# Kernel optimization log

Measured on AMD Instinct MI355X. Metric: run time of the kernel, lower is better.

## Reference

```python
import jax, jax.numpy as jnp
import numpy as np

EPS = 1e-6


def setup_inputs() -> dict:
    key = jax.random.key(0)
    ks = jax.random.split(key, 10)
    N1, N2, K, E, LAYERS = 4096, 4096, 10, 262144, 3
    D = 2 ** K  # 1024
    us = jax.random.uniform(ks[0], (LAYERS, N1, D), dtype=jnp.float32)
    vs = jax.random.uniform(ks[1], (LAYERS, N2, D), dtype=jnp.float32)
    gamma = jax.random.normal(ks[2], (N1, LAYERS), dtype=jnp.float32)
    delta = jax.random.normal(ks[3], (N2, LAYERS), dtype=jnp.float32)
    latent_z1 = jax.random.uniform(ks[4], (N1, LAYERS), dtype=jnp.float32)
    latent_w1 = jax.random.uniform(ks[5], (N2, LAYERS), dtype=jnp.float32)
    # p_k_l initialized as log(uniform) in torch; any real values are valid params
    p_ks = jnp.full((LAYERS, K + 1), jnp.log(1.0 / (K + 1)), dtype=jnp.float32)
    p_ks = p_ks + 0.01 * jax.random.normal(ks[6], (LAYERS, K + 1), dtype=jnp.float32)
    L_ = 5.0 * jnp.ones((1,), dtype=jnp.float32)
    sparse_is = jax.random.randint(ks[7], (LAYERS, E), 0, N1, dtype=jnp.int64) if jax.config.jax_enable_x64 else jax.random.randint(ks[7], (LAYERS, E), 0, N1).astype(jnp.int32)
    sparse_js = jax.random.randint(ks[8], (LAYERS, E), 0, N2).astype(sparse_is.dtype)
    return {"us": us, "vs": vs, "gamma": gamma, "delta": delta,
            "latent_z1": latent_z1, "latent_w1": latent_w1,
            "p_ks": p_ks, "L_": L_,
            "sparse_is": sparse_is, "sparse_js": sparse_js}


def reference(us, vs, gamma, delta, latent_z1, latent_w1, p_ks, L_, sparse_is, sparse_js):
    LAYERS, N1, D = us.shape
    N2 = vs.shape[1]
    K = p_ks.shape[1] - 1  # tree_height
    latent_z = jax.nn.softmax(latent_z1, axis=1)  # Softmax(dim=1)
    latent_w = jax.nn.softmax(latent_w1, axis=1)
    L = jax.nn.softplus(L_)[0]
    ll = jnp.float32(0.0)
    for layer in range(LAYERS):
        p_k = jax.nn.softmax(p_ks[layer], axis=0)  # soft_0
        g = gamma[:, layer]                         # [N1]
        d = delta[:, layer]                         # [N2]
        emb_z = jax.nn.softmax(us[layer], axis=1)   # [N1, D]
        emb_w = jax.nn.softmax(vs[layer], axis=1)   # [N2, D]
        # hierarchical tree-weighted similarity: sum of GEMMs at coarsening levels
        inter = p_k[0] * jnp.ones((N1, N2), dtype=us.dtype)
        z_k, w_k = emb_z, emb_w
        for k in range(1, K):
            z_k = z_k.reshape(N1, -1, 2).sum(axis=2)  # [N1, D/2^k]
            w_k = w_k.reshape(N2, -1, 2).sum(axis=2)  # [N2, D/2^k]
            inter = inter + p_k[k] * jnp.einsum('nd,md->nm', z_k, w_k + EPS)
        inter = inter + p_k[K] * jnp.einsum('nd,md->nm', emb_z, emb_w + EPS)
        mat_1 = g[:, None] + d[None, :]                              # [N1, N2]
        mat_0 = (latent_z[:, layer][:, None] * L) * (latent_w[:, layer] + EPS)[None, :] * inter
        mat = jax.nn.softplus(mat_0 + mat_1)
        z_pdist1 = mat.sum()
        if N1 == N2:  # remove diagonal contributions
            z_pdist1 = z_pdist1 - jnp.trace(mat)
        i_ = sparse_is[layer]
        j_ = sparse_js[layer]
        z_pdist2 = (mat_0[i_, j_] + mat_1[i_, j_]).sum()
        ll = ll + (z_pdist2 - z_pdist1)
    return ll
```

## Files before the change

kernel.cpp:

```cpp
#include <hip/hip_runtime.h>
#include <hip/hip_bf16.h>
#include <stdint.h>

#define EPSV 1e-6f
#define N1 4096
#define N2 4096
#define DD 1024
#define NLAYERS 3
#define KKC 10

typedef __bf16 bf16_t;
typedef __bf16 bf16x8 __attribute__((ext_vector_type(8)));
typedef float f32x4 __attribute__((ext_vector_type(4)));
typedef long longx2 __attribute__((ext_vector_type(2)));

#define ZSCALE 256.0f
#define WSCALE 64.0f
#define INVSCALE 6.103515625e-05f

#define NBIN_L 1024
#define NBIN_T (NLAYERS*NBIN_L)

__device__ __forceinline__ float softplus_fast(float x) {
  return fmaxf(x, 0.f) + __logf(1.f + __expf(-fabsf(x)));
}
__device__ __forceinline__ float softplus_ref(float x) {
  return fmaxf(x, 0.f) + log1pf(expf(-fabsf(x)));
}
__device__ __forceinline__ float wredsum(float x) {
  #pragma unroll
  for (int o = 32; o; o >>= 1) x += __shfl_xor(x, o, 64);
  return x;
}
__device__ __forceinline__ float wredmax(float x) {
  #pragma unroll
  for (int o = 32; o; o >>= 1) x = fmaxf(x, __shfl_xor(x, o, 64));
  return x;
}
__device__ __forceinline__ void global_load_lds16(const void* g, void* l) {
  __builtin_amdgcn_global_load_lds(
      (const __attribute__((address_space(1))) uint32_t*)g,
      (__attribute__((address_space(3))) uint32_t*)l, 16, 0, 0);
}

__device__ __forceinline__ uint32_t enc_e4m3(float x) {
  if (x < 0.015625f) return (uint32_t)__float2int_rn(x * 512.0f);
  uint32_t u = __float_as_uint(x);
  u += 0x7FFFFu + ((u >> 20) & 1u);
  return (((u >> 23) - 120u) << 3) | ((u >> 20) & 7u);
}

__global__ __launch_bounds__(256) void prep_small(
    const float* __restrict__ lz, const float* __restrict__ lw,
    const float* __restrict__ gamma, const float* __restrict__ delta,
    const float* __restrict__ pks, const float* __restrict__ Lp,
    float* __restrict__ consts, float* __restrict__ a_tab, float* __restrict__ b_tab,
    float* __restrict__ g_tab, float* __restrict__ d_tab,
    uint32_t* __restrict__ hist, float* __restrict__ out)
{
  int n = blockIdx.x * blockDim.x + threadIdx.x;
  float Lv = softplus_ref(Lp[0]);
  if (n == 0) out[0] = 0.f;
  if (n < NBIN_T) hist[n] = 0u;
  if (n < N1) {
    float z0 = lz[n*3], z1 = lz[n*3+1], z2 = lz[n*3+2];
    float m = fmaxf(z0, fmaxf(z1, z2));
    float e0 = expf(z0-m), e1 = expf(z1-m), e2 = expf(z2-m);
    float inv = 1.f/(e0+e1+e2);
    a_tab[0*N1+n] = e0*inv*Lv; a_tab[1*N1+n] = e1*inv*Lv; a_tab[2*N1+n] = e2*inv*Lv;
    float w0 = lw[n*3], w1 = lw[n*3+1], w2 = lw[n*3+2];
    m = fmaxf(w0, fmaxf(w1, w2));
    e0 = expf(w0-m); e1 = expf(w1-m); e2 = expf(w2-m);
    inv = 1.f/(e0+e1+e2);
    b_tab[0*N2+n] = e0*inv+EPSV; b_tab[1*N2+n] = e1*inv+EPSV; b_tab[2*N2+n] = e2*inv+EPSV;
    #pragma unroll
    for (int k = 0; k < 3; ++k) {
      g_tab[k*N1+n] = gamma[n*3+k];
      d_tab[k*N2+n] = delta[n*3+k];
    }
  }
  if (n < NLAYERS) {
    float p[KKC+1]; float m = -1e30f;
    for (int k = 0; k <= KKC; ++k) { p[k] = pks[n*(KKC+1)+k]; m = fmaxf(m, p[k]); }
    float s = 0.f;
    for (int k = 0; k <= KKC; ++k) { p[k] = expf(p[k]-m); s += p[k]; }
    float inv = 1.f/s;
    for (int k = 0; k <= KKC; ++k) consts[8 + n*(KKC+1) + k] = p[k]*inv;
    consts[n] = p[0]*inv + EPSV*(1.f - p[0]*inv);
  }
}

#define EPB 2048

__global__ __launch_bounds__(256) void edge_hist(
    const int* __restrict__ is_, const int* __restrict__ js_,
    uint32_t* __restrict__ hist, int E)
{
  __shared__ uint32_t h[NBIN_L];
  const int lay = blockIdx.y;
  const int t = threadIdx.x;
  #pragma unroll
  for (int i = 0; i < NBIN_L/256; ++i) h[t + i*256] = 0u;
  __syncthreads();
  const int e0 = blockIdx.x * EPB;
  const int e1 = min(e0 + EPB, E);
  for (int e = e0 + t; e < e1; e += 256) {
    int i = is_[(size_t)lay*E + e], j = js_[(size_t)lay*E + e];
    atomicAdd(&h[(i>>7)*32 + (j>>7)], 1u);
  }
  __syncthreads();
  #pragma unroll
  for (int i = 0; i < NBIN_L/256; ++i)
    if (h[t + i*256]) atomicAdd(&hist[lay*NBIN_L + t + i*256], h[t + i*256]);
}

__global__ __launch_bounds__(256) void edge_scan(
    const uint32_t* __restrict__ hist, uint32_t* __restrict__ off,
    uint32_t* __restrict__ cursor, int E)
{
  __shared__ uint32_t sa[NBIN_L], sb[NBIN_L];
  const int lay = blockIdx.x;
  const int t = threadIdx.x;
  const uint32_t base = (uint32_t)lay * (uint32_t)E;
  for (int i = t; i < NBIN_L; i += 256) sa[i] = hist[lay*NBIN_L + i];
  __syncthreads();
  uint32_t* src = sa; uint32_t* dst = sb;
  for (int s = 1; s < NBIN_L; s <<= 1) {
    for (int i = t; i < NBIN_L; i += 256) dst[i] = src[i] + (i >= s ? src[i-s] : 0u);
    __syncthreads();
    uint32_t* tmp = src; src = dst; dst = tmp;
  }
  for (int i = t; i < NBIN_L; i += 256) {
    uint32_t ex = base + (i ? src[i-1] : 0u);
    off[lay*NBIN_L + i] = ex; cursor[lay*NBIN_L + i] = ex;
  }
  if (t == 0 && lay == NLAYERS-1) off[NBIN_T] = base + src[NBIN_L-1];
}

__global__ __launch_bounds__(256) void edge_scatter(
    const int* __restrict__ is_, const int* __restrict__ js_,
    uint32_t* __restrict__ cursor, uint16_t* __restrict__ ebuf, int E)
{
  __shared__ uint32_t h[NBIN_L];
  __shared__ uint32_t basev[NBIN_L];
  const int lay = blockIdx.y;
  const int t = threadIdx.x;
  #pragma unroll
  for (int i = 0; i < NBIN_L/256; ++i) h[t + i*256] = 0u;
  __syncthreads();
  const int e0 = blockIdx.x * EPB;
  const int e1 = min(e0 + EPB, E);
  for (int e = e0 + t; e < e1; e += 256) {
    int i = is_[(size_t)lay*E + e], j = js_[(size_t)lay*E + e];
    atomicAdd(&h[(i>>7)*32 + (j>>7)], 1u);
  }
  __syncthreads();
  #pragma unroll
  for (int i = 0; i < NBIN_L/256; ++i) {
    int b = t + i*256;
    basev[b] = h[b] ? atomicAdd(&cursor[lay*NBIN_L + b], h[b]) : 0u;
    h[b] = 0u;
  }
  __syncthreads();
  for (int e = e0 + t; e < e1; e += 256) {
    int i = is_[(size_t)lay*E + e], j = js_[(size_t)lay*E + e];
    int b = (i>>7)*32 + (j>>7);
    uint32_t r = atomicAdd(&h[b], 1u);
    ebuf[basev[b] + r] = (uint16_t)(((i & 127) << 7) | (j & 127));
  }
}

__global__ __launch_bounds__(256) void prep_rows(
    const float* __restrict__ us, const float* __restrict__ vs,
    uint8_t* __restrict__ zt8, uint8_t* __restrict__ wt8, size_t lstride,
    const float* __restrict__ consts, int layer0)
{
  const int t = threadIdx.x, w = t >> 6, l = t & 63;
  const int n = blockIdx.x*4 + w;
  const int layer = layer0 + blockIdx.y;
  const int zmode = (blockIdx.z == 0);
  const float* src = (zmode ? us : vs) + ((size_t)layer*N1 + n)*DD + l*16;
  uint8_t* drow = (zmode ? zt8 : wt8) + (size_t)blockIdx.y*lstride + (size_t)n*1024;
  const int p0 = (l>>2)*64 + ((l&1)*2)*16 + ((l&3)>>1)*8;

  float e[16];
  {
    const float4* s4 = (const float4*)src;
    float4 u0 = s4[0], u1 = s4[1], u2 = s4[2], u3 = s4[3];
    e[0]=u0.x; e[1]=u0.y; e[2]=u0.z; e[3]=u0.w;
    e[4]=u1.x; e[5]=u1.y; e[6]=u1.z; e[7]=u1.w;
    e[8]=u2.x; e[9]=u2.y; e[10]=u2.z; e[11]=u2.w;
    e[12]=u3.x; e[13]=u3.y; e[14]=u3.z; e[15]=u3.w;
  }
  float mx = e[0];
  #pragma unroll
  for (int i = 1; i < 16; ++i) mx = fmaxf(mx, e[i]);
  mx = wredmax(mx);
  float s = 0.f;
  #pragma unroll
  for (int i = 0; i < 16; ++i) { e[i] = __expf(e[i]-mx); s += e[i]; }
  s = wredsum(s);
  float inv = 1.f/s;
  #pragma unroll
  for (int i = 0; i < 16; ++i) e[i] *= inv;

  uint32_t b4[4] = {0u, 0u, 0u, 0u};
  if (!zmode) {
    #pragma unroll
    for (int i = 0; i < 16; ++i)
      b4[i>>2] |= enc_e4m3(e[i]*WSCALE) << ((i&3)*8);
  } else {
    float s1[8], s2[4], s3[2], s4v;
    #pragma unroll
    for (int i = 0; i < 8; ++i) s1[i] = e[2*i] + e[2*i+1];
    #pragma unroll
    for (int i = 0; i < 4; ++i) s2[i] = s1[2*i] + s1[2*i+1];
    s3[0] = s2[0]+s2[1]; s3[1] = s2[2]+s2[3];
    s4v = s3[0]+s3[1];
    float s5 = s4v + __shfl_xor(s4v, 1, 64);
    float s6 = s5  + __shfl_xor(s5, 2, 64);
    float s7 = s6  + __shfl_xor(s6, 4, 64);
    float s8 = s7  + __shfl_xor(s7, 8, 64);
    float s9 = s8  + __shfl_xor(s8, 16, 64);
    const float* pk = consts + 8 + layer*(KKC+1);
    const float base = pk[4]*s4v + pk[5]*s5 + pk[6]*s6 + pk[7]*s7 + pk[8]*s8 + pk[9]*s9;
    const float p1 = pk[1], p2 = pk[2], p3 = pk[3], p10 = pk[10];
    #pragma unroll
    for (int i = 0; i < 16; ++i) {
      float v = p10*e[i] + p1*s1[i>>1] + p2*s2[i>>2] + p3*s3[i>>3] + base;
      b4[i>>2] |= enc_e4m3(v*ZSCALE) << ((i&3)*8);
    }
  }
  uint64_t u0 = (uint64_t)b4[0] | ((uint64_t)b4[1] << 32);
  uint64_t u1 = (uint64_t)b4[2] | ((uint64_t)b4[3] << 32);
  *(uint64_t*)(drow + p0)      = u0;
  *(uint64_t*)(drow + p0 + 16) = u1;
}

__global__ __launch_bounds__(256, 4) void gemm_fused(
    const uint8_t* __restrict__ Az8, size_t zls,
    const uint8_t* __restrict__ Bw8, size_t wls,
    const float* __restrict__ a_tab, const float* __restrict__ b_tab,
    const float* __restrict__ g_tab, const float* __restrict__ d_tab,
    const float* __restrict__ consts, int layer0,
    const uint32_t* __restrict__ eoff, const uint16_t* __restrict__ ebuf,
    float* __restrict__ out)
{
  extern __shared__ char lds[];
  const int t = threadIdx.x;
  const int w = t >> 6, l = t & 63;
  const int wm = w >> 1, wn = w & 1;
  const int fr = l & 15, fq = l >> 4;

  const int nbx = gridDim.x, nby = gridDim.y;
  int lid = blockIdx.x + nbx*(blockIdx.y + nby*blockIdx.z);
  const int nblk = nbx*nby*gridDim.z;
  const int cpx = nblk >> 3;
  int nid = (lid & 7)*cpx + (lid >> 3);
  const int bz = nid / (nbx*nby);
  const int rem = nid % (nbx*nby);
  const int bi = rem % nbx, bj = rem / nbx;

  const int i0 = bi*128, j0 = bj*128;
  const int layer = layer0 + bz;
  Az8 += (size_t)bz*zls + (size_t)i0*1024;
  Bw8 += (size_t)bz*wls + (size_t)j0*1024;

  f32x4 acc[4][4];
  f32x4 zero = {0.f, 0.f, 0.f, 0.f};
  #pragma unroll
  for (int m = 0; m < 4; ++m)
    #pragma unroll
    for (int nn = 0; nn < 4; ++nn) acc[m][nn] = zero;

  const int go = (l & 7) ^ (l >> 3);
  const size_t s_off = (size_t)((l >> 3)*2 + (go >> 2))*1024 + (size_t)(go & 3)*16;
  const int slot = (((fr & 1) << 2) + fq) ^ (fr >> 1);
  const int abase = wm*4096 + (fr>>1)*128 + slot*16;
  const int bbase = 8192 + wn*4096 + (fr>>1)*128 + slot*16;

  longx2 ar2[4], br2[4];

#define STG_A(tile) do { \
    char* _d = lds + ((tile)&1)*16384 + w*2048; \
    const uint8_t* _s = Az8 + (size_t)(w*32)*1024 + (size_t)(tile)*64 + s_off; \
    global_load_lds16(_s, _d); \
    global_load_lds16(_s + (size_t)16*1024, _d + 1024); \
  } while (0)
#define STG_B(tile) do { \
    char* _d = lds + ((tile)&1)*16384 + 8192 + w*2048; \
    const uint8_t* _s = Bw8 + (size_t)(w*32)*1024 + (size_t)(tile)*64 + s_off; \
    global_load_lds16(_s, _d); \
    global_load_lds16(_s + (size_t)16*1024, _d + 1024); \
  } while (0)

  STG_A(0); STG_B(0);

  for (int u = 0; u < 16; ++u) {
    const int cb = (u & 1)*16384;
    asm volatile("s_waitcnt vmcnt(0)" ::: "memory");
    asm volatile("s_barrier" ::: "memory");
    #pragma unroll
    for (int i = 0; i < 4; ++i)
      ar2[i] = *(const longx2*)(lds + cb + abase + i*1024);
    #pragma unroll
    for (int j = 0; j < 4; ++j)
      br2[j] = *(const longx2*)(lds + cb + bbase + j*1024);
    if (u < 15) { STG_A(u+1); STG_B(u+1); }
    __builtin_amdgcn_s_setprio(1);
    #pragma unroll
    for (int i = 0; i < 4; ++i)
      #pragma unroll
      for (int j = 0; j < 4; ++j) {
        acc[i][j] = __builtin_amdgcn_mfma_f32_16x16x32_fp8_fp8(
            ar2[i].x, br2[j].x, acc[i][j], 0, 0, 0);
        acc[i][j] = __builtin_amdgcn_mfma_f32_16x16x32_fp8_fp8(
            ar2[i].y, br2[j].y, acc[i][j], 0, 0, 0);
      }
    __builtin_amdgcn_s_setprio(0);
  }
#undef STG_A
#undef STG_B

  __syncthreads();
  const float cc = consts[layer];
  {
    char* cbase = lds + wm*16384 + fq*1024 + wn*128 + fr*2;
    #pragma unroll
    for (int m = 0; m < 4; ++m)
      #pragma unroll
      for (int nn = 0; nn < 4; ++nn)
        #pragma unroll
        for (int r = 0; r < 4; ++r)
          *(bf16_t*)(cbase + m*4096 + r*256 + nn*32) =
              (bf16_t)(acc[m][nn][r]*INVSCALE + cc);
  }
  __syncthreads();

  const float* at = a_tab + layer*N1;
  const float* bt = b_tab + layer*N2;
  const float* gt = g_tab + layer*N1;
  const float* dt = d_tab + layer*N2;
  float dsum = 0.f;
  #pragma unroll
  for (int i = 0; i < 8; ++i) {
    const int id = t + i*256;
    const int row = id >> 4, g = id & 15;
    bf16x8 v = *(const bf16x8*)(lds + row*256 + g*16);
    const int grow = i0 + row, gcol = j0 + g*8;
    const float av = at[grow], gv = gt[grow];
    float4 b0 = *(const float4*)(bt + gcol), b1 = *(const float4*)(bt + gcol + 4);
    float4 d0 = *(const float4*)(dt + gcol), d1 = *(const float4*)(dt + gcol + 4);
    float bb[8] = {b0.x,b0.y,b0.z,b0.w,b1.x,b1.y,b1.z,b1.w};
    float dd[8] = {d0.x,d0.y,d0.z,d0.w,d1.x,d1.y,d1.z,d1.w};
    #pragma unroll
    for (int e2 = 0; e2 < 8; ++e2) {
      float x = av*bb[e2]*(float)v[e2] + gv + dd[e2];
      float sp = softplus_fast(x);
      dsum += (grow != gcol + e2) ? sp : 0.f;
    }
  }
  const int bin = bz*NBIN_L + bi*32 + bj;
  const uint32_t e0 = eoff[bin], e1 = eoff[bin+1];
  float ssum = 0.f;
  for (uint32_t e = e0 + (uint32_t)t; e < e1; e += 256u) {
    const int pk2 = ebuf[e];
    const int li = pk2 >> 7, lj = pk2 & 127;
    float dc = (float)*(const bf16_t*)(lds + li*256 + lj*2);
    ssum += at[i0+li]*bt[j0+lj]*dc + gt[i0+li] + dt[j0+lj];
  }
  float tot = wredsum(ssum - dsum);
  __syncthreads();
  if (l == 0) ((float*)lds)[w] = tot;
  __syncthreads();
  if (t == 0) {
    const float* r = (const float*)lds;
    atomicAdd(out, r[0] + r[1] + r[2] + r[3]);
  }
}

extern "C" void kernel_launch(void* const* d_in, const int* in_sizes, int n_in,
                              void* d_out, int out_size, void* d_ws, size_t ws_size,
                              hipStream_t stream) {
  const float* us    = (const float*)d_in[0];
  const float* vs    = (const float*)d_in[1];
  const float* gamma = (const float*)d_in[2];
  const float* delta = (const float*)d_in[3];
  const float* lz    = (const float*)d_in[4];
  const float* lw    = (const float*)d_in[5];
  const float* pks   = (const float*)d_in[6];
  const float* Lp    = (const float*)d_in[7];
  const int*   sis   = (const int*)d_in[8];
  const int*   sjs   = (const int*)d_in[9];
  float* out = (float*)d_out;
  char*  ws  = (char*)d_ws;
  const int E = in_sizes[8] / NLAYERS;

  size_t p = 0;
  float* consts = (float*)(ws + p); p += 1024;
  float* a_tab  = (float*)(ws + p); p += (size_t)NLAYERS*N1*4;
  float* b_tab  = (float*)(ws + p); p += (size_t)NLAYERS*N2*4;
  float* g_tab  = (float*)(ws + p); p += (size_t)NLAYERS*N1*4;
  float* d_tab  = (float*)(ws + p); p += (size_t)NLAYERS*N2*4;
  uint32_t* hist   = (uint32_t*)(ws + p); p += 4096*4;
  uint32_t* eoff   = (uint32_t*)(ws + p); p += 4096*4;
  uint32_t* cursor = (uint32_t*)(ws + p); p += 4096*4;
  uint16_t* ebuf   = (uint16_t*)(ws + p); p += (size_t)NLAYERS*E*2;
  p = (p + 4095) & ~(size_t)4095;
  uint8_t* zt8 = (uint8_t*)(ws + p); p += (size_t)NLAYERS*N1*1024;
  uint8_t* wt8 = (uint8_t*)(ws + p); p += (size_t)NLAYERS*N2*1024;
  if (ws_size < p) return;
  const size_t ZLS = (size_t)N1*1024;
  const size_t LDSB = 32768;
  const int nebl = (E + EPB - 1) / EPB;

  prep_small<<<(N1+255)/256, 256, 0, stream>>>(lz, lw, gamma, delta, pks, Lp,
                                               consts, a_tab, b_tab, g_tab, d_tab,
                                               hist, out);
  edge_hist<<<dim3(nebl, NLAYERS), 256, 0, stream>>>(sis, sjs, hist, E);
  edge_scan<<<NLAYERS, 256, 0, stream>>>(hist, eoff, cursor, E);
  edge_scatter<<<dim3(nebl, NLAYERS), 256, 0, stream>>>(sis, sjs, cursor, ebuf, E);
  prep_rows<<<dim3(N1/4, NLAYERS, 2), 256, 0, stream>>>(us, vs, zt8, wt8, ZLS, consts, 0);
  gemm_fused<<<dim3(32,32,NLAYERS), 256, LDSB, stream>>>(
      zt8, ZLS, wt8, ZLS, a_tab, b_tab, g_tab, d_tab, consts, 0, eoff, ebuf, out);
}
```

Before: 132.8 us.

## Load A tiles directly to registers, stage only B through LDS

The fp8 GEMM now loads A fragments straight from global memory into double-buffered registers instead of staging them through LDS, which halves the LDS buffer footprint and LDS read traffic. The block-to-tile mapping is transposed so consecutive blocks share the same rows of A, and the loop is fully unrolled. Launch bounds drop from 4 to 3 waves per SIMD to give room for the extra registers. The cost is more VGPR pressure, lower occupancy, and uncoalesced per-lane global loads for A.

```diff
diff --git a/kernel.cpp b/kernel.cpp
--- a/kernel.cpp
+++ b/kernel.cpp
@@ -237,7 +237,7 @@
   *(uint64_t*)(drow + p0 + 16) = u1;
 }
 
-__global__ __launch_bounds__(256, 4) void gemm_fused(
+__global__ __launch_bounds__(256, 3) void gemm_fused(
     const uint8_t* __restrict__ Az8, size_t zls,
     const uint8_t* __restrict__ Bw8, size_t wls,
     const float* __restrict__ a_tab, const float* __restrict__ b_tab,
@@ -259,7 +259,7 @@
   int nid = (lid & 7)*cpx + (lid >> 3);
   const int bz = nid / (nbx*nby);
   const int rem = nid % (nbx*nby);
-  const int bi = rem % nbx, bj = rem / nbx;
+  const int bj = rem % nby, bi = rem / nby;
 
   const int i0 = bi*128, j0 = bj*128;
   const int layer = layer0 + bz;
@@ -276,51 +276,52 @@
   const int go = (l & 7) ^ (l >> 3);
   const size_t s_off = (size_t)((l >> 3)*2 + (go >> 2))*1024 + (size_t)(go & 3)*16;
   const int slot = (((fr & 1) << 2) + fq) ^ (fr >> 1);
-  const int abase = wm*4096 + (fr>>1)*128 + slot*16;
-  const int bbase = 8192 + wn*4096 + (fr>>1)*128 + slot*16;
-
-  longx2 ar2[4], br2[4];
-
-#define STG_A(tile) do { \
-    char* _d = lds + ((tile)&1)*16384 + w*2048; \
-    const uint8_t* _s = Az8 + (size_t)(w*32)*1024 + (size_t)(tile)*64 + s_off; \
-    global_load_lds16(_s, _d); \
-    global_load_lds16(_s + (size_t)16*1024, _d + 1024); \
-  } while (0)
+  const int bbase = wn*4096 + (fr>>1)*128 + slot*16;
+
+  const uint8_t* pA = Az8 + (size_t)(wm*64 + fr)*1024 + (size_t)fq*16;
+
+  longx2 ar[2][4], br2[4];
+
 #define STG_B(tile) do { \
-    char* _d = lds + ((tile)&1)*16384 + 8192 + w*2048; \
+    char* _d = lds + ((tile)&1)*8192 + w*2048; \
     const uint8_t* _s = Bw8 + (size_t)(w*32)*1024 + (size_t)(tile)*64 + s_off; \
     global_load_lds16(_s, _d); \
     global_load_lds16(_s + (size_t)16*1024, _d + 1024); \
   } while (0)
-
-  STG_A(0); STG_B(0);
-
+#define LOAD_A(buf, tile) do { \
+    _Pragma("unroll") for (int m = 0; m < 4; ++m) \
+      ar[buf][m] = *(const longx2*)(pA + (size_t)m*16384 + (size_t)(tile)*64); \
+  } while (0)
+
+  STG_B(0);
+  LOAD_A(0, 0);
+
+  #pragma unroll
   for (int u = 0; u < 16; ++u) {
-    const int cb = (u & 1)*16384;
+    const int cb = (u & 1)*8192;
     asm volatile("s_waitcnt vmcnt(0)" ::: "memory");
     asm volatile("s_barrier" ::: "memory");
-    #pragma unroll
-    for (int i = 0; i < 4; ++i)
-      ar2[i] = *(const longx2*)(lds + cb + abase + i*1024);
+    if (u < 15) {
+      STG_B(u+1);
+      LOAD_A((u+1)&1, u+1);
+    }
     #pragma unroll
     for (int j = 0; j < 4; ++j)
       br2[j] = *(const longx2*)(lds + cb + bbase + j*1024);
-    if (u < 15) { STG_A(u+1); STG_B(u+1); }
     __builtin_amdgcn_s_setprio(1);
     #pragma unroll
     for (int i = 0; i < 4; ++i)
       #pragma unroll
       for (int j = 0; j < 4; ++j) {
         acc[i][j] = __builtin_amdgcn_mfma_f32_16x16x32_fp8_fp8(
-            ar2[i].x, br2[j].x, acc[i][j], 0, 0, 0);
+            ar[u&1][i].x, br2[j].x, acc[i][j], 0, 0, 0);
         acc[i][j] = __builtin_amdgcn_mfma_f32_16x16x32_fp8_fp8(
-            ar2[i].y, br2[j].y, acc[i][j], 0, 0, 0);
+            ar[u&1][i].y, br2[j].y, acc[i][j], 0, 0, 0);
       }
     __builtin_amdgcn_s_setprio(0);
   }
-#undef STG_A
 #undef STG_B
+#undef LOAD_A
 
   __syncthreads();
   const float cc = consts[layer];
```

Result: slower. 175.7 us (+32.3%).
